# Performance work log

Measured on AMD Instinct MI355X. Metric: run time of the kernel, lower is better.

Reference implementation:

```python
import jax, jax.numpy as jnp
import numpy as np

B, T, I, H, O = 128, 1024, 1, 512, 1


def setup_inputs() -> dict:
    key = jax.random.key(0)
    k = jax.random.split(key, 6)
    s = 1.0 / np.sqrt(H).astype(np.float32)
    x = jax.random.normal(k[0], (B, T, I), dtype=jnp.float32)
    Wx = jax.random.uniform(k[1], (I, 4 * H), jnp.float32, -s, s)   # input->gates
    Wh = jax.random.uniform(k[2], (H, 4 * H), jnp.float32, -s, s)   # hidden->gates
    b = jax.random.uniform(k[3], (4 * H,), jnp.float32, -s, s)      # gate bias
    Wl = jax.random.uniform(k[4], (H, O), jnp.float32, -s, s)       # readout
    bl = jax.random.uniform(k[5], (O,), jnp.float32, -s, s)
    return {"x": x, "Wx": Wx, "Wh": Wh, "b": b, "Wl": Wl, "bl": bl, "future": 0}


def reference(x, Wx, Wh, b, Wl, bl, future):
    # x: (B, T, I). Custom LSTM cell unrolled over time via lax.scan, with a
    # per-timestep linear readout (as in the original per-step loop).
    H_ = Wh.shape[0]
    h0 = jnp.zeros((x.shape[0], H_), dtype=x.dtype)
    c0 = jnp.zeros((x.shape[0], H_), dtype=x.dtype)

    def step(carry, xt):  # xt: (B, I)
        h, c = carry
        gates = xt @ Wx + h @ Wh + b            # (B, 4H)
        i, f, g, o = jnp.split(gates, 4, axis=-1)
        i = jax.nn.sigmoid(i)
        f = jax.nn.sigmoid(f)
        g = jnp.tanh(g)
        o = jax.nn.sigmoid(o)
        c = f * c + i * g
        h = o * jnp.tanh(c)
        y = h @ Wl + bl                          # (B, O)
        return (h, c), y

    (_, _), ys = jax.lax.scan(step, (h0, c0), jnp.swapaxes(x, 0, 1))
    # ys: (T, B, O) -> (B, T, O), matching torch.stack(outputs,1).squeeze(2)
    return jnp.swapaxes(ys, 0, 1)
```

## Files before the change

### kernel.cpp

```cpp
#include <hip/hip_runtime.h>
#include <hip/hip_fp16.h>


typedef _Float16 f16;
typedef _Float16 f16x8 __attribute__((ext_vector_type(8)));
typedef float f32x4 __attribute__((ext_vector_type(4)));

#define BATCH 128
#define TT 1024
#define HID 512

#define WPACK_OFF   0
#define WPACK_BYTES (32*4*16*64*16)
#define HBUF_OFF    WPACK_BYTES
#define HBUF_ELEMS  (BATCH*HID)
#define WL16_OFF    (HBUF_OFF + 4*HBUF_ELEMS*2)
#define HHIST_OFF   (WL16_OFF + 4096)
#define HHIST_BYTES ((size_t)TT * BATCH * HID * 2)
#define WS_NEEDED   ((size_t)HHIST_OFF + HHIST_BYTES)

__global__ __launch_bounds__(256) void init_kernel(const float* Wl, f16* wl16,
                                                   unsigned* hbuf) {
    int idx = blockIdx.x * 256 + threadIdx.x;
    hbuf[idx] = ((idx >> 15) == 0) ? 0u : 0x00010001u;
    if (idx < HID) wl16[idx] = (f16)Wl[idx];
}

__global__ __launch_bounds__(256) void pack_kernel(const float* __restrict__ Wh,
                                                   f16* __restrict__ wpack) {
    int tid  = blockIdx.x * 256 + threadIdx.x;
    int lane = tid & 63;
    int s    = (tid >> 6) & 15;
    int wv   = (tid >> 10) & 3;
    int cg   = tid >> 12;
    int l_lo = lane & 15, l_hi = lane >> 4;
    int jt = ((wv * 4) + s) & 15;
    int jj = l_lo >> 2, q = l_lo & 3;
    int c = q * 512 + cg * 16 + wv * 4 + jj;
    int kbase = jt * 32 + l_hi * 8;
    f16x8 v;
#pragma unroll
    for (int e = 0; e < 8; ++e) v[e] = (f16)Wh[(kbase + e) * 2048 + c];
    ((f16x8*)wpack)[tid] = v;
}

__device__ __forceinline__ float dot8(f16x8 a, f16x8 b, float acc) {
#if __has_builtin(__builtin_amdgcn_fdot2)
    acc = __builtin_amdgcn_fdot2(__builtin_shufflevector(a, a, 0, 1),
                                 __builtin_shufflevector(b, b, 0, 1), acc, false);
    acc = __builtin_amdgcn_fdot2(__builtin_shufflevector(a, a, 2, 3),
                                 __builtin_shufflevector(b, b, 2, 3), acc, false);
    acc = __builtin_amdgcn_fdot2(__builtin_shufflevector(a, a, 4, 5),
                                 __builtin_shufflevector(b, b, 4, 5), acc, false);
    acc = __builtin_amdgcn_fdot2(__builtin_shufflevector(a, a, 6, 7),
                                 __builtin_shufflevector(b, b, 6, 7), acc, false);
#else
#pragma unroll
    for (int e = 0; e < 8; ++e) acc += (float)a[e] * (float)b[e];
#endif
    return acc;
}

template<int CTRL>
__device__ __forceinline__ float dpp_qp(float v) {
    int r = __builtin_amdgcn_update_dpp(0, __builtin_bit_cast(int, v),
                                        CTRL, 0xF, 0xF, true);
    return __builtin_bit_cast(float, r);
}

template<int MODE>
__global__ __launch_bounds__(256, 1) void lstm_kernel(
    const float* __restrict__ x, const float* __restrict__ Wx,
    const float* __restrict__ bvec, const float* __restrict__ blp,
    const f16* __restrict__ wpack, f16* __restrict__ hbuf,
    const f16* __restrict__ wl16, f16* __restrict__ hhist,
    float* __restrict__ out)
{
    const int tid = threadIdx.x;
    const int cg = blockIdx.x >> 3;
    const int bg = blockIdx.x & 7;
    const int w = tid >> 6, lane = tid & 63;
    const int l_lo = lane & 15, l_hi = lane >> 4;

    __shared__ f16 hsh[2][8192];
    __shared__ f16 wlsh[512];

    if (tid < 64)
        *(f16x8*)(wlsh + tid * 8) = *(const f16x8*)(wl16 + tid * 8);

    f16x8 bf[16];
    {
        const f16x8* wp = (const f16x8*)wpack + (size_t)((cg * 4 + w) * 16) * 64 + lane;
#pragma unroll
        for (int s = 0; s < 16; ++s) bf[s] = wp[s * 64];
    }

    const int row  = l_hi * 4 + (l_lo & 3);
    const int uglob = cg * 16 + w * 4 + (l_lo >> 2);
    const int bglob = bg * 16 + row;
    const float bias_i = bvec[0*512+uglob], bias_f = bvec[1*512+uglob];
    const float bias_g = bvec[2*512+uglob], bias_o = bvec[3*512+uglob];
    const float wx_i = Wx[0*512+uglob], wx_f = Wx[1*512+uglob];
    const float wx_g = Wx[2*512+uglob], wx_o = Wx[3*512+uglob];
    const float blv = blp[0];

    const int rd_base = bg * 8192 + ((w * 16 + l_hi) * 16 + l_lo) * 8;
    const int st_idx = bg * 8192 + ((uglob >> 3) * 16 + row) * 8 + (uglob & 7);
    const int hist_off = (bg * 16 + row) * 512 + uglob;

    const int p4 = l_lo & 3;
    const int sx = (l_lo & 7) << 4;
    const int lbase = l_lo * 1024;
    const int base_ws = w * 256 + l_hi * 16;
    const int xrow = bglob * TT;

    float cst = 0.f;
    const int TLAST = (MODE == 0) ? (TT - 1) : TT;

    for (int t = 0; t <= TLAST; ++t) {
        const f16* hp = hbuf + (size_t)(t & 3) * HBUF_ELEMS + rd_base;
        const unsigned ep = (unsigned)((t >> 2) & 1) * 0x00010001u;
        float xv = x[xrow + (t < TT ? t : 0)];

        f16x8 s0, s1, s2, s3;
        for (;;) {
            asm volatile(
                "global_load_dwordx4 %0, %4, off sc0 sc1\n\t"
                "global_load_dwordx4 %1, %5, off sc0 sc1\n\t"
                "global_load_dwordx4 %2, %6, off sc0 sc1\n\t"
                "global_load_dwordx4 %3, %7, off sc0 sc1\n\t"
                "s_waitcnt vmcnt(0)"
                : "=&v"(s0), "=&v"(s1), "=&v"(s2), "=&v"(s3)
                : "v"(hp), "v"(hp + 512), "v"(hp + 1024), "v"(hp + 1536)
                : "memory");
            union { f16x8 v; unsigned u[4]; } b0, b1, b2, b3;
            b0.v = s0; b1.v = s1; b2.v = s2; b3.v = s3;
            unsigned bad =
                (((b0.u[0]^ep)|(b0.u[1]^ep)|(b0.u[2]^ep)|(b0.u[3]^ep)) |
                 ((b1.u[0]^ep)|(b1.u[1]^ep)|(b1.u[2]^ep)|(b1.u[3]^ep)) |
                 ((b2.u[0]^ep)|(b2.u[1]^ep)|(b2.u[2]^ep)|(b2.u[3]^ep)) |
                 ((b3.u[0]^ep)|(b3.u[1]^ep)|(b3.u[2]^ep)|(b3.u[3]^ep))) & 0x00010001u;
            if (__all(bad == 0u)) break;
        }
        __builtin_amdgcn_sched_barrier(0);

        char* hb = (char*)hsh[t & 1];
        const int wb = lbase + base_ws;
        *(f16x8*)(hb + ((wb +   0) ^ sx)) = s0;
        *(f16x8*)(hb + ((wb +  64) ^ sx)) = s1;
        *(f16x8*)(hb + ((wb + 128) ^ sx)) = s2;
        *(f16x8*)(hb + ((wb + 192) ^ sx)) = s3;

        f32x4 c0 = {0,0,0,0};
        if (t < TT) {
            c0 = __builtin_amdgcn_mfma_f32_16x16x32_f16(s0, bf[0], c0, 0,0,0);
            c0 = __builtin_amdgcn_mfma_f32_16x16x32_f16(s1, bf[1], c0, 0,0,0);
            c0 = __builtin_amdgcn_mfma_f32_16x16x32_f16(s2, bf[2], c0, 0,0,0);
            c0 = __builtin_amdgcn_mfma_f32_16x16x32_f16(s3, bf[3], c0, 0,0,0);
        }
        __syncthreads();

        if (t < TT) {
            f32x4 c1 = {0,0,0,0}, c2 = {0,0,0,0}, c3 = {0,0,0,0};
#pragma unroll
            for (int i = 0; i < 4; ++i) {
                f16x8 a1 = *(const f16x8*)(hb + ((lbase + ((base_ws + (4+i)*64) & 1023)) ^ sx));
                f16x8 a2 = *(const f16x8*)(hb + ((lbase + ((base_ws + (8+i)*64) & 1023)) ^ sx));
                f16x8 a3 = *(const f16x8*)(hb + ((lbase + ((base_ws + (12+i)*64) & 1023)) ^ sx));
                c1 = __builtin_amdgcn_mfma_f32_16x16x32_f16(a1, bf[ 4+i], c1, 0,0,0);
                c2 = __builtin_amdgcn_mfma_f32_16x16x32_f16(a2, bf[ 8+i], c2, 0,0,0);
                c3 = __builtin_amdgcn_mfma_f32_16x16x32_f16(a3, bf[12+i], c3, 0,0,0);
            }
            f32x4 m = (c0 + c1) + (c2 + c3);

            float t0, e0, e1, e2, e3, f0, f1, f2, f3;
            t0 = dpp_qp<0xB1>(m[1]); e0 = (p4 & 1) ? t0 : m[0];
            t0 = dpp_qp<0xB1>(m[0]); e1 = (p4 & 1) ? m[1] : t0;
            t0 = dpp_qp<0xB1>(m[3]); e2 = (p4 & 1) ? t0 : m[2];
            t0 = dpp_qp<0xB1>(m[2]); e3 = (p4 & 1) ? m[3] : t0;
            t0 = dpp_qp<0x4E>(e2); f0 = (p4 & 2) ? t0 : e0;
            t0 = dpp_qp<0x4E>(e3); f1 = (p4 & 2) ? t0 : e1;
            t0 = dpp_qp<0x4E>(e0); f2 = (p4 & 2) ? e2 : t0;
            t0 = dpp_qp<0x4E>(e1); f3 = (p4 & 2) ? e3 : t0;

            float gi = f0 + xv * wx_i + bias_i;
            float gf = f1 + xv * wx_f + bias_f;
            float gg = f2 + xv * wx_g + bias_g;
            float go = f3 + xv * wx_o + bias_o;
            float iv = 1.f / (1.f + __expf(-gi));
            float fv = 1.f / (1.f + __expf(-gf));
            float gv = 2.f / (1.f + __expf(-2.f * gg)) - 1.f;
            float ov = 1.f / (1.f + __expf(-go));
            cst = fv * cst + iv * gv;
            float hv = ov * (2.f / (1.f + __expf(-2.f * cst)) - 1.f);

            unsigned hval;
            { union { f16 f; unsigned short s; } cv; cv.f = (f16)hv; hval = cv.s; }

            if ((MODE == 0) ? (t < TT - 1) : true) {
                const unsigned wtag = (unsigned)(((t + 1) >> 2) & 1);
                unsigned tagged = (hval & 0xFFFEu) | wtag;
                f16* dst = hbuf + (size_t)((t + 1) & 3) * HBUF_ELEMS + st_idx;
                asm volatile("global_store_short %0, %1, off sc0 sc1"
                             :: "v"(dst), "v"(tagged) : "memory");
            }

            if (MODE == 0) {
                f16* hd = hhist + (size_t)t * (BATCH * HID) + hist_off;
                asm volatile("global_store_short %0, %1, off"
                             :: "v"(hd), "v"(hval) : "memory");
            }
        }

        if (MODE == 1 && t >= 1 && cg == ((t >> 2) & 31) && w == (t & 3)) {
            float r0 = 0.f, r1 = 0.f, r2 = 0.f, r3 = 0.f;
#define WL(s) (*(const f16x8*)(wlsh + (((base_ws + (s)*64) & 1023) >> 1)))
            r0 = dot8(s0, WL(0), r0);
            r1 = dot8(s1, WL(1), r1);
            r2 = dot8(s2, WL(2), r2);
            r3 = dot8(s3, WL(3), r3);
#pragma unroll
            for (int i = 0; i < 4; ++i) {
                f16x8 a1 = *(const f16x8*)(hb + ((lbase + ((base_ws + (4+i)*64) & 1023)) ^ sx));
                f16x8 a2 = *(const f16x8*)(hb + ((lbase + ((base_ws + (8+i)*64) & 1023)) ^ sx));
                f16x8 a3 = *(const f16x8*)(hb + ((lbase + ((base_ws + (12+i)*64) & 1023)) ^ sx));
                r0 = dot8(a1, WL(4+i),  r0);
                r1 = dot8(a2, WL(8+i),  r1);
                r2 = dot8(a3, WL(12+i), r2);
            }
#undef WL
            float ry = (r0 + r1) + (r2 + r3);
            ry += __shfl_xor(ry, 16);
            ry += __shfl_xor(ry, 32);
            if (lane < 16)
                out[(bg * 16 + l_lo) * TT + (t - 1)] = blv + ry;
        }
    }
}

__global__ __launch_bounds__(256) void readout_kernel(
    const f16* __restrict__ hhist, const float* __restrict__ Wl,
    const float* __restrict__ blp, float* __restrict__ out)
{
    int gw = (blockIdx.x * 256 + threadIdx.x) >> 6;
    int lane = threadIdx.x & 63;
    int b = gw >> 7;
    int t0 = (gw & 127) * 8;
    const float4* wp = (const float4*)(Wl + lane * 8);
    float4 wa = wp[0], wb = wp[1];
    float blv = blp[0];
    const f16* hp = hhist + (size_t)t0 * (BATCH * HID) + b * HID + lane * 8;
#pragma unroll
    for (int j = 0; j < 8; ++j) {
        f16x8 h8 = *(const f16x8*)(hp + (size_t)j * (BATCH * HID));
        float p = (float)h8[0]*wa.x + (float)h8[1]*wa.y + (float)h8[2]*wa.z +
                  (float)h8[3]*wa.w + (float)h8[4]*wb.x + (float)h8[5]*wb.y +
                  (float)h8[6]*wb.z + (float)h8[7]*wb.w;
        p += __shfl_xor(p, 1);  p += __shfl_xor(p, 2);  p += __shfl_xor(p, 4);
        p += __shfl_xor(p, 8);  p += __shfl_xor(p, 16); p += __shfl_xor(p, 32);
        if (lane == 0) out[b * TT + t0 + j] = p + blv;
    }
}

extern "C" void kernel_launch(void* const* d_in, const int* in_sizes, int n_in,
                              void* d_out, int out_size, void* d_ws, size_t ws_size,
                              hipStream_t stream) {
    const float* x  = (const float*)d_in[0];
    const float* Wx = (const float*)d_in[1];
    const float* Wh = (const float*)d_in[2];
    const float* bv = (const float*)d_in[3];
    const float* Wl = (const float*)d_in[4];
    const float* bl = (const float*)d_in[5];
    float* out = (float*)d_out;
    char* ws = (char*)d_ws;

    f16* wpack = (f16*)(ws + WPACK_OFF);
    f16* hbuf  = (f16*)(ws + HBUF_OFF);
    f16* wl16  = (f16*)(ws + WL16_OFF);
    f16* hhist = (f16*)(ws + HHIST_OFF);

    init_kernel<<<512, 256, 0, stream>>>(Wl, wl16, (unsigned*)hbuf);
    pack_kernel<<<512, 256, 0, stream>>>(Wh, wpack);
    if (ws_size >= WS_NEEDED) {
        lstm_kernel<0><<<256, 256, 0, stream>>>(x, Wx, bv, bl, wpack, hbuf,
                                                wl16, hhist, out);
        readout_kernel<<<4096, 256, 0, stream>>>(hhist, Wl, bl, out);
    } else {
        lstm_kernel<1><<<256, 256, 0, stream>>>(x, Wx, bv, bl, wpack, hbuf,
                                                wl16, hhist, out);
    }
}
```

Baseline: 1.915 ms.

## Halve LSTM grid so each wave computes two hidden-unit tiles per step

Each block now owns 32 hidden units instead of 16, so the persistent LSTM kernel launches 128 blocks instead of 256. The Wh packing adds a tile dimension, and each wave holds two sets of weight fragments and runs twice the MFMAs against the same loaded h fragments. The aim is to cut the number of blocks spinning on the cross-block h exchange each timestep and reuse each h load across more output columns. The cost is double the per-wave MFMA and activation work on a serial path, plus many more registers (32 f16x8 weight fragments), which risks spilling.

```diff
diff --git a/kernel.cpp b/kernel.cpp
--- a/kernel.cpp
+++ b/kernel.cpp
@@ -11,7 +11,7 @@
 #define HID 512
 
 #define WPACK_OFF   0
-#define WPACK_BYTES (32*4*16*64*16)
+#define WPACK_BYTES (16*4*2*16*64*16)
 #define HBUF_OFF    WPACK_BYTES
 #define HBUF_ELEMS  (BATCH*HID)
 #define WL16_OFF    (HBUF_OFF + 4*HBUF_ELEMS*2)
@@ -31,12 +31,13 @@
     int tid  = blockIdx.x * 256 + threadIdx.x;
     int lane = tid & 63;
     int s    = (tid >> 6) & 15;
-    int wv   = (tid >> 10) & 3;
-    int cg   = tid >> 12;
+    int T    = (tid >> 10) & 1;
+    int wv   = (tid >> 11) & 3;
+    int cg   = tid >> 13;
     int l_lo = lane & 15, l_hi = lane >> 4;
     int jt = ((wv * 4) + s) & 15;
     int jj = l_lo >> 2, q = l_lo & 3;
-    int c = q * 512 + cg * 16 + wv * 4 + jj;
+    int c = q * 512 + cg * 32 + T * 16 + wv * 4 + jj;
     int kbase = jt * 32 + l_hi * 8;
     f16x8 v;
 #pragma unroll
@@ -66,6 +67,20 @@
     int r = __builtin_amdgcn_update_dpp(0, __builtin_bit_cast(int, v),
                                         CTRL, 0xF, 0xF, true);
     return __builtin_bit_cast(float, r);
+}
+
+__device__ __forceinline__ void quad_transpose(const f32x4& m, int p4,
+                                               float& f0, float& f1,
+                                               float& f2, float& f3) {
+    float t0, e0, e1, e2, e3;
+    t0 = dpp_qp<0xB1>(m[1]); e0 = (p4 & 1) ? t0 : m[0];
+    t0 = dpp_qp<0xB1>(m[0]); e1 = (p4 & 1) ? m[1] : t0;
+    t0 = dpp_qp<0xB1>(m[3]); e2 = (p4 & 1) ? t0 : m[2];
+    t0 = dpp_qp<0xB1>(m[2]); e3 = (p4 & 1) ? m[3] : t0;
+    t0 = dpp_qp<0x4E>(e2); f0 = (p4 & 2) ? t0 : e0;
+    t0 = dpp_qp<0x4E>(e3); f1 = (p4 & 2) ? t0 : e1;
+    t0 = dpp_qp<0x4E>(e0); f2 = (p4 & 2) ? e2 : t0;
+    t0 = dpp_qp<0x4E>(e1); f3 = (p4 & 2) ? e3 : t0;
 }
 
 template<int MODE>
@@ -88,25 +103,35 @@
     if (tid < 64)
         *(f16x8*)(wlsh + tid * 8) = *(const f16x8*)(wl16 + tid * 8);
 
-    f16x8 bf[16];
+    f16x8 bf0[16], bf1[16];
     {
-        const f16x8* wp = (const f16x8*)wpack + (size_t)((cg * 4 + w) * 16) * 64 + lane;
-#pragma unroll
-        for (int s = 0; s < 16; ++s) bf[s] = wp[s * 64];
+        const f16x8* wp0 = (const f16x8*)wpack
+                         + (size_t)(((cg * 4 + w) * 2 + 0) * 16) * 64 + lane;
+        const f16x8* wp1 = (const f16x8*)wpack
+                         + (size_t)(((cg * 4 + w) * 2 + 1) * 16) * 64 + lane;
+#pragma unroll
+        for (int s = 0; s < 16; ++s) { bf0[s] = wp0[s * 64]; bf1[s] = wp1[s * 64]; }
     }
 
     const int row  = l_hi * 4 + (l_lo & 3);
-    const int uglob = cg * 16 + w * 4 + (l_lo >> 2);
+    const int u0 = cg * 32 + w * 4 + (l_lo >> 2);
+    const int u1 = u0 + 16;
     const int bglob = bg * 16 + row;
-    const float bias_i = bvec[0*512+uglob], bias_f = bvec[1*512+uglob];
-    const float bias_g = bvec[2*512+uglob], bias_o = bvec[3*512+uglob];
-    const float wx_i = Wx[0*512+uglob], wx_f = Wx[1*512+uglob];
-    const float wx_g = Wx[2*512+uglob], wx_o = Wx[3*512+uglob];
+    const float bi0 = bvec[0*512+u0], bfo0 = bvec[1*512+u0];
+    const float bg0 = bvec[2*512+u0], bo0 = bvec[3*512+u0];
+    const float bi1 = bvec[0*512+u1], bfo1 = bvec[1*512+u1];
+    const float bg1 = bvec[2*512+u1], bo1 = bvec[3*512+u1];
+    const float wxi0 = Wx[0*512+u0], wxf0 = Wx[1*512+u0];
+    const float wxg0 = Wx[2*512+u0], wxo0 = Wx[3*512+u0];
+    const float wxi1 = Wx[0*512+u1], wxf1 = Wx[1*512+u1];
+    const float wxg1 = Wx[2*512+u1], wxo1 = Wx[3*512+u1];
     const float blv = blp[0];
 
     const int rd_base = bg * 8192 + ((w * 16 + l_hi) * 16 + l_lo) * 8;
-    const int st_idx = bg * 8192 + ((uglob >> 3) * 16 + row) * 8 + (uglob & 7);
-    const int hist_off = (bg * 16 + row) * 512 + uglob;
+    const int st_idx0 = bg * 8192 + ((u0 >> 3) * 16 + row) * 8 + (u0 & 7);
+    const int st_idx1 = bg * 8192 + ((u1 >> 3) * 16 + row) * 8 + (u1 & 7);
+    const int hist0 = (bg * 16 + row) * 512 + u0;
+    const int hist1 = (bg * 16 + row) * 512 + u1;
 
     const int p4 = l_lo & 3;
     const int sx = (l_lo & 7) << 4;
@@ -114,7 +139,7 @@
     const int base_ws = w * 256 + l_hi * 16;
     const int xrow = bglob * TT;
 
-    float cst = 0.f;
+    float cst0 = 0.f, cst1 = 0.f;
     const int TLAST = (MODE == 0) ? (TT - 1) : TT;
 
     for (int t = 0; t <= TLAST; ++t) {
@@ -151,68 +176,85 @@
         *(f16x8*)(hb + ((wb + 128) ^ sx)) = s2;
         *(f16x8*)(hb + ((wb + 192) ^ sx)) = s3;
 
-        f32x4 c0 = {0,0,0,0};
+        f32x4 cA0 = {0,0,0,0}, cA1 = {0,0,0,0};
         if (t < TT) {
-            c0 = __builtin_amdgcn_mfma_f32_16x16x32_f16(s0, bf[0], c0, 0,0,0);
-            c0 = __builtin_amdgcn_mfma_f32_16x16x32_f16(s1, bf[1], c0, 0,0,0);
-            c0 = __builtin_amdgcn_mfma_f32_16x16x32_f16(s2, bf[2], c0, 0,0,0);
-            c0 = __builtin_amdgcn_mfma_f32_16x16x32_f16(s3, bf[3], c0, 0,0,0);
+            cA0 = __builtin_amdgcn_mfma_f32_16x16x32_f16(s0, bf0[0], cA0, 0,0,0);
+            cA1 = __builtin_amdgcn_mfma_f32_16x16x32_f16(s0, bf1[0], cA1, 0,0,0);
+            cA0 = __builtin_amdgcn_mfma_f32_16x16x32_f16(s1, bf0[1], cA0, 0,0,0);
+            cA1 = __builtin_amdgcn_mfma_f32_16x16x32_f16(s1, bf1[1], cA1, 0,0,0);
+            cA0 = __builtin_amdgcn_mfma_f32_16x16x32_f16(s2, bf0[2], cA0, 0,0,0);
+            cA1 = __builtin_amdgcn_mfma_f32_16x16x32_f16(s2, bf1[2], cA1, 0,0,0);
+            cA0 = __builtin_amdgcn_mfma_f32_16x16x32_f16(s3, bf0[3], cA0, 0,0,0);
+            cA1 = __builtin_amdgcn_mfma_f32_16x16x32_f16(s3, bf1[3], cA1, 0,0,0);
         }
         __syncthreads();
 
         if (t < TT) {
-            f32x4 c1 = {0,0,0,0}, c2 = {0,0,0,0}, c3 = {0,0,0,0};
+            f32x4 cB0 = {0,0,0,0}, cB1 = {0,0,0,0};
+            f32x4 cC0 = {0,0,0,0}, cC1 = {0,0,0,0};
+            f32x4 cD0 = {0,0,0,0}, cD1 = {0,0,0,0};
 #pragma unroll
             for (int i = 0; i < 4; ++i) {
                 f16x8 a1 = *(const f16x8*)(hb + ((lbase + ((base_ws + (4+i)*64) & 1023)) ^ sx));
                 f16x8 a2 = *(const f16x8*)(hb + ((lbase + ((base_ws + (8+i)*64) & 1023)) ^ sx));
                 f16x8 a3 = *(const f16x8*)(hb + ((lbase + ((base_ws + (12+i)*64) & 1023)) ^ sx));
-                c1 = __builtin_amdgcn_mfma_f32_16x16x32_f16(a1, bf[ 4+i], c1, 0,0,0);
-                c2 = __builtin_amdgcn_mfma_f32_16x16x32_f16(a2, bf[ 8+i], c2, 0,0,0);
-                c3 = __builtin_amdgcn_mfma_f32_16x16x32_f16(a3, bf[12+i], c3, 0,0,0);
+                cB0 = __builtin_amdgcn_mfma_f32_16x16x32_f16(a1, bf0[ 4+i], cB0, 0,0,0);
+                cB1 = __builtin_amdgcn_mfma_f32_16x16x32_f16(a1, bf1[ 4+i], cB1, 0,0,0);
+                cC0 = __builtin_amdgcn_mfma_f32_16x16x32_f16(a2, bf0[ 8+i], cC0, 0,0,0);
+                cC1 = __builtin_amdgcn_mfma_f32_16x16x32_f16(a2, bf1[ 8+i], cC1, 0,0,0);
+                cD0 = __builtin_amdgcn_mfma_f32_16x16x32_f16(a3, bf0[12+i], cD0, 0,0,0);
+                cD1 = __builtin_amdgcn_mfma_f32_16x16x32_f16(a3, bf1[12+i], cD1, 0,0,0);
             }
-            f32x4 m = (c0 + c1) + (c2 + c3);
-
-            float t0, e0, e1, e2, e3, f0, f1, f2, f3;
-            t0 = dpp_qp<0xB1>(m[1]); e0 = (p4 & 1) ? t0 : m[0];
-            t0 = dpp_qp<0xB1>(m[0]); e1 = (p4 & 1) ? m[1] : t0;
-            t0 = dpp_qp<0xB1>(m[3]); e2 = (p4 & 1) ? t0 : m[2];
-            t0 = dpp_qp<0xB1>(m[2]); e3 = (p4 & 1) ? m[3] : t0;
-            t0 = dpp_qp<0x4E>(e2); f0 = (p4 & 2) ? t0 : e0;
-            t0 = dpp_qp<0x4E>(e3); f1 = (p4 & 2) ? t0 : e1;
-            t0 = dpp_qp<0x4E>(e0); f2 = (p4 & 2) ? e2 : t0;
-            t0 = dpp_qp<0x4E>(e1); f3 = (p4 & 2) ? e3 : t0;
-
-            float gi = f0 + xv * wx_i + bias_i;
-            float gf = f1 + xv * wx_f + bias_f;
-            float gg = f2 + xv * wx_g + bias_g;
-            float go = f3 + xv * wx_o + bias_o;
-            float iv = 1.f / (1.f + __expf(-gi));
-            float fv = 1.f / (1.f + __expf(-gf));
-            float gv = 2.f / (1.f + __expf(-2.f * gg)) - 1.f;
-            float ov = 1.f / (1.f + __expf(-go));
-            cst = fv * cst + iv * gv;
-            float hv = ov * (2.f / (1.f + __expf(-2.f * cst)) - 1.f);
-
-            unsigned hval;
-            { union { f16 f; unsigned short s; } cv; cv.f = (f16)hv; hval = cv.s; }
+            f32x4 m0 = (cA0 + cB0) + (cC0 + cD0);
+            f32x4 m1 = (cA1 + cB1) + (cC1 + cD1);
+
+            float gi0, gf0, gg0, go0, gi1, gf1, gg1, go1;
+            quad_transpose(m0, p4, gi0, gf0, gg0, go0);
+            quad_transpose(m1, p4, gi1, gf1, gg1, go1);
+
+            gi0 += xv * wxi0 + bi0;  gf0 += xv * wxf0 + bfo0;
+            gg0 += xv * wxg0 + bg0;  go0 += xv * wxo0 + bo0;
+            gi1 += xv * wxi1 + bi1;  gf1 += xv * wxf1 + bfo1;
+            gg1 += xv * wxg1 + bg1;  go1 += xv * wxo1 + bo1;
+
+            float iv0 = 1.f / (1.f + __expf(-gi0));
+            float fv0 = 1.f / (1.f + __expf(-gf0));
+            float gv0 = 2.f / (1.f + __expf(-2.f * gg0)) - 1.f;
+            float ov0 = 1.f / (1.f + __expf(-go0));
+            float iv1 = 1.f / (1.f + __expf(-gi1));
+            float fv1 = 1.f / (1.f + __expf(-gf1));
+            float gv1 = 2.f / (1.f + __expf(-2.f * gg1)) - 1.f;
+            float ov1 = 1.f / (1.f + __expf(-go1));
+            cst0 = fv0 * cst0 + iv0 * gv0;
+            cst1 = fv1 * cst1 + iv1 * gv1;
+            float hv0 = ov0 * (2.f / (1.f + __expf(-2.f * cst0)) - 1.f);
+            float hv1 = ov1 * (2.f / (1.f + __expf(-2.f * cst1)) - 1.f);
+
+            unsigned h0, h1;
+            { union { f16 f; unsigned short s; } cv;
+              cv.f = (f16)hv0; h0 = cv.s; cv.f = (f16)hv1; h1 = cv.s; }
 
             if ((MODE == 0) ? (t < TT - 1) : true) {
                 const unsigned wtag = (unsigned)(((t + 1) >> 2) & 1);
-                unsigned tagged = (hval & 0xFFFEu) | wtag;
-                f16* dst = hbuf + (size_t)((t + 1) & 3) * HBUF_ELEMS + st_idx;
+                unsigned tg0 = (h0 & 0xFFFEu) | wtag;
+                unsigned tg1 = (h1 & 0xFFFEu) | wtag;
+                f16* dstb = hbuf + (size_t)((t + 1) & 3) * HBUF_ELEMS;
                 asm volatile("global_store_short %0, %1, off sc0 sc1"
-                             :: "v"(dst), "v"(tagged) : "memory");
+                             :: "v"(dstb + st_idx0), "v"(tg0) : "memory");
+                asm volatile("global_store_short %0, %1, off sc0 sc1"
+                             :: "v"(dstb + st_idx1), "v"(tg1) : "memory");
             }
 
             if (MODE == 0) {
-                f16* hd = hhist + (size_t)t * (BATCH * HID) + hist_off;
+                f16* hd = hhist + (size_t)t * (BATCH * HID);
                 asm volatile("global_store_short %0, %1, off"
-                             :: "v"(hd), "v"(hval) : "memory");
+                             :: "v"(hd + hist0), "v"(h0) : "memory");
+                asm volatile("global_store_short %0, %1, off"
+                             :: "v"(hd + hist1), "v"(h1) : "memory");
             }
         }
 
-        if (MODE == 1 && t >= 1 && cg == ((t >> 2) & 31) && w == (t & 3)) {
+        if (MODE == 1 && t >= 1 && cg == ((t >> 2) & 15) && w == (t & 3)) {
             float r0 = 0.f, r1 = 0.f, r2 = 0.f, r3 = 0.f;
 #define WL(s) (*(const f16x8*)(wlsh + (((base_ws + (s)*64) & 1023) >> 1)))
             r0 = dot8(s0, WL(0), r0);
@@ -282,11 +324,11 @@
     init_kernel<<<512, 256, 0, stream>>>(Wl, wl16, (unsigned*)hbuf);
     pack_kernel<<<512, 256, 0, stream>>>(Wh, wpack);
     if (ws_size >= WS_NEEDED) {
-        lstm_kernel<0><<<256, 256, 0, stream>>>(x, Wx, bv, bl, wpack, hbuf,
+        lstm_kernel<0><<<128, 256, 0, stream>>>(x, Wx, bv, bl, wpack, hbuf,
                                                 wl16, hhist, out);
         readout_kernel<<<4096, 256, 0, stream>>>(hhist, Wl, bl, out);
     } else {
-        lstm_kernel<1><<<256, 256, 0, stream>>>(x, Wx, bv, bl, wpack, hbuf,
+        lstm_kernel<1><<<128, 256, 0, stream>>>(x, Wx, bv, bl, wpack, hbuf,
                                                 wl16, hhist, out);
     }
 }
```

New measurement: 1.850 ms. 1.04x faster.
